# Performance work log

Measured on AMD Instinct MI355X. Metric: run time of the kernel, lower is better.

The kernel has to match this reference:

```python
import jax, jax.numpy as jnp
import numpy as np

N_NODES = 524288
N_EDGES = 786432
NUM_GRAPHS = 8192
NUM_NODE_TYPES = 16
NODE_DIM = 256
EDGE_DIM = 128
OUT_DIM = 1


def setup_inputs() -> dict:
    key = jax.random.key(0)
    ks = jax.random.split(key, 12)
    h_node = jax.random.uniform(ks[0], (N_NODES, NUM_NODE_TYPES), dtype=jnp.float32)
    pos_node = jax.random.normal(ks[1], (N_NODES, 3), dtype=jnp.float32)
    batch_node = jnp.sort(jax.random.randint(ks[2], (N_NODES,), 0, NUM_GRAPHS)).astype(jnp.int64)
    edge_index = jax.random.randint(ks[3], (2, N_EDGES), 0, N_NODES).astype(jnp.int64)
    batch_edge = jnp.sort(jax.random.randint(ks[4], (N_EDGES,), 0, NUM_GRAPHS)).astype(jnp.int64)
    s = 0.05
    W_node = jax.random.normal(ks[5], (NUM_NODE_TYPES, NODE_DIM), dtype=jnp.float32) * s
    W_edge = jax.random.normal(ks[6], (2 * NUM_NODE_TYPES, EDGE_DIM), dtype=jnp.float32) * s
    H = NODE_DIM + EDGE_DIM
    W1 = jax.random.normal(ks[7], (H, H), dtype=jnp.float32) * s
    b1 = jnp.zeros((H,), dtype=jnp.float32)
    W2 = jax.random.normal(ks[8], (H, OUT_DIM), dtype=jnp.float32) * s
    b2 = jnp.zeros((OUT_DIM,), dtype=jnp.float32)
    return {"h_node": h_node, "pos_node": pos_node, "batch_node": batch_node,
            "edge_index": edge_index, "batch_edge": batch_edge,
            "W_node": W_node, "W_edge": W_edge, "W1": W1, "b1": b1, "W2": W2, "b2": b2}


def _segment_mean(x, seg_ids, num_segments):
    # fused replacement for the original per-graph boolean-mask loop:
    # h[seg==k].mean(0) for all k, via one scatter-add + count normalize
    sums = jax.ops.segment_sum(x, seg_ids, num_segments=num_segments)
    cnts = jax.ops.segment_sum(jnp.ones((x.shape[0],), x.dtype), seg_ids, num_segments=num_segments)
    return sums / jnp.maximum(cnts, 1.0)[:, None]


def reference(h_node, pos_node, batch_node, edge_index, batch_edge,
              W_node, W_edge, W1, b1, W2, b2):
    # h_edge = cat(h_node[src], h_node[dst])  -> [E, 2*num_node_types]
    h_edge_raw = jnp.concatenate([h_node[edge_index[0]], h_node[edge_index[1]]], axis=-1)
    # num_timesteps == 0 path: plain embedders, no time embedding
    hn = h_node @ W_node          # [N, node_dim]
    he = h_edge_raw @ W_edge      # [E, edge_dim]
    # encoder treated as identity (NodeEdgeNet not in scope); pooling is the target op
    node_mean = _segment_mean(hn, batch_node, NUM_GRAPHS)  # [G, node_dim]
    edge_mean = _segment_mean(he, batch_edge, NUM_GRAPHS)  # [G, edge_dim]
    h_sub = jnp.concatenate([node_mean, edge_mean], axis=-1)  # [G, node_dim+edge_dim]
    # final MLP (num_layer=2): Linear -> ReLU -> Linear
    pred = jax.nn.relu(h_sub @ W1 + b1) @ W2 + b2  # [G, 1]
    return pred
```

## Files before the change

### kernel.cpp

```cpp
#include <hip/hip_runtime.h>

#define N_NODES_C   524288
#define N_EDGES_C   786432
#define NUM_GRAPHS_C 8192
#define NT 16
#define NODE_DIM_C 256
#define EDGE_DIM_C 128
#define HDIM 384
#define KC 48

#define FOLD_BLOCKS 72
#define NODE_BLOCKS 2048
#define EDGE_BLOCKS 16384
#define NODE_BASE   FOLD_BLOCKS
#define EDGE_BASE   (FOLD_BLOCKS + NODE_BLOCKS)
#define TOTAL_BLOCKS (FOLD_BLOCKS + NODE_BLOCKS + EDGE_BLOCKS)

#define WS_NM    0
#define WS_EM    524288
#define WS_WC    1572864
#define WS_NS    1646592
#define WS_BOFF  1679424
#define WS_ECNT  2203712
#define WS_REC   2236480

__device__ __forceinline__ void f4_add(float4& a, const float4 v) {
    a.x += v.x; a.y += v.y; a.z += v.z; a.w += v.w;
}

__device__ __forceinline__ void f4_shfl_xor_add(float4& a, int mask) {
    a.x += __shfl_xor(a.x, mask, 64);
    a.y += __shfl_xor(a.y, mask, 64);
    a.z += __shfl_xor(a.z, mask, 64);
    a.w += __shfl_xor(a.w, mask, 64);
}

__device__ __forceinline__ int lower_bound_i32(const int* __restrict__ a, int n, int key) {
    int lo = 0, hi = n;
    while (lo < hi) {
        int mid = (lo + hi) >> 1;
        if (a[mid] < key) lo = mid + 1; else hi = mid;
    }
    return lo;
}

__device__ __forceinline__ void wave_seg_bounds(const int* __restrict__ b, int n,
                                                int g, int lane, int& s, int& e) {
    int key = g + ((lane >= 32) ? 1 : 0);
    int lo = lower_bound_i32(b, n, key);
    s = __shfl(lo, 0, 64);
    e = __shfl(lo, 32, 64);
}

__global__ __launch_bounds__(256) void kr_build(
    const int* __restrict__ bnode, const int* __restrict__ bedge,
    const int* __restrict__ esrc, const int* __restrict__ edst,
    int* __restrict__ rec, int* __restrict__ binoff,
    int* __restrict__ ecnt, int* __restrict__ nstart, float* __restrict__ em) {
    int tid = threadIdx.x, blk = blockIdx.x;
    int i = blk * 256 + tid;
    {
        int g0 = bnode[i];
        int hi = (i + 1 < N_NODES_C) ? bnode[i + 1] : NUM_GRAPHS_C;
        if (i == 0) for (int g = 0; g <= g0; ++g) nstart[g] = 0;
        for (int g = g0 + 1; g <= hi; ++g) nstart[g] = i + 1;
    }
    if (tid < 128) em[blk * 128 + tid] = 0.f;

    int wave = tid >> 6, lane = tid & 63;
    int g = blk * 4 + wave;
    int s, e;
    wave_seg_bounds(bedge, N_EDGES_C, g, lane, s, e);
    if (lane == 0) ecnt[g] = e - s;

    __shared__ int lcnt[4][16];
    __shared__ int lcur[4][16];
    if (lane < 16) lcnt[wave][lane] = 0;
    for (int q = s + lane; q < e; q += 64) {
        int a = esrc[q];
        atomicAdd(&lcnt[wave][((a >> 16) << 1) + 0], 1);
        int b = edst[q];
        atomicAdd(&lcnt[wave][((b >> 16) << 1) + 1], 1);
    }
    int c = (lane < 16) ? lcnt[wave][lane] : 0;
    int incl = c;
    #pragma unroll
    for (int d = 1; d < 16; d <<= 1) {
        int v = __shfl_up(incl, d, 64);
        if (lane >= d) incl += v;
    }
    int excl = incl - c;
    if (lane < 16) {
        lcur[wave][lane] = excl;
        binoff[g * 16 + lane] = 2 * s + excl;
    }
    for (int q = s + lane; q < e; q += 64) {
        int a = esrc[q];
        int pa = atomicAdd(&lcur[wave][((a >> 16) << 1) + 0], 1);
        rec[2 * s + pa] = a;
        int b = edst[q];
        int pb = atomicAdd(&lcur[wave][((b >> 16) << 1) + 1], 1);
        rec[2 * s + pb] = b;
    }
}

__global__ __launch_bounds__(256) void km_mega(
    const float* __restrict__ h_node,
    const int* __restrict__ nstart, const int* __restrict__ binoff,
    const int* __restrict__ ecnt, const int* __restrict__ rec,
    const float* __restrict__ Wn, const float* __restrict__ We,
    const float* __restrict__ W1,
    float* __restrict__ nm, float* __restrict__ em, float* __restrict__ Wc) {
    int blk  = blockIdx.x;
    int wave = threadIdx.x >> 6;
    int lane = threadIdx.x & 63;
    const float4* h4 = (const float4*)h_node;
    const float4 z4 = make_float4(0.f, 0.f, 0.f, 0.f);

    if (blk < FOLD_BLOCKS) {
        int o = blk * 256 + threadIdx.x;
        if (o >= KC * HDIM) return;
        int k = o / HDIM, j = o % HDIM;
        float acc = 0.f;
        if (k < NT) {
            const float* wr = &Wn[k * NODE_DIM_C];
            #pragma unroll 16
            for (int kk = 0; kk < NODE_DIM_C; ++kk)
                acc = fmaf(wr[kk], W1[(size_t)kk * HDIM + j], acc);
        } else {
            const float* wr = &We[(k - NT) * EDGE_DIM_C];
            #pragma unroll 16
            for (int kk = 0; kk < EDGE_DIM_C; ++kk)
                acc = fmaf(wr[kk], W1[(size_t)(NODE_DIM_C + kk) * HDIM + j], acc);
        }
        Wc[o] = acc;
    } else if (blk < EDGE_BASE) {
        int r = blk - NODE_BASE;
        int s8 = r & 7;
        int g  = s8 * 1024 + (r >> 3) * 4 + wave;
        int s = nstart[g], e = nstart[g + 1];
        int row_off = lane >> 2;
        int quad    = lane & 3;
        float4 a0 = z4, a1 = z4;
        int i = s + row_off;
        for (; i + 16 < e; i += 32) {
            float4 v0 = h4[(size_t)i * 4 + quad];
            float4 v1 = h4[(size_t)(i + 16) * 4 + quad];
            f4_add(a0, v0);
            f4_add(a1, v1);
        }
        if (i < e) f4_add(a0, h4[(size_t)i * 4 + quad]);
        f4_add(a0, a1);
        f4_shfl_xor_add(a0, 4);
        f4_shfl_xor_add(a0, 8);
        f4_shfl_xor_add(a0, 16);
        f4_shfl_xor_add(a0, 32);
        if (row_off == 0) {
            float inv = 1.f / fmaxf((float)(e - s), 1.f);
            ((float4*)nm)[(size_t)g * 4 + quad] =
                make_float4(a0.x * inv, a0.y * inv, a0.z * inv, a0.w * inv);
        }
    } else {
        int r     = blk - EDGE_BASE;
        int slice = r & 7;
        int g     = (r >> 3) * 4 + wave;
        int b16   = g * 16 + slice * 2;
        int base0 = binoff[b16];
        int base1 = binoff[b16 + 1];
        int cnt   = ecnt[g];
        int end1  = (slice == 7) ? binoff[g * 16] + 2 * cnt : binoff[b16 + 2];
        int slot = lane >> 3;
        int p    = (lane >> 2) & 1;
        int quad = lane & 3;
        int st = p ? base1 : base0;
        int en = p ? end1  : base1;
        int cmax = max(base1 - base0, end1 - base1);
        int T = (cmax + 7) >> 3;
        float4 acc = z4;
        int i = st + slot;
        int idx = (i < en) ? rec[i] : -1;
        for (int t = 1; t < T; ++t) {
            int i2 = i + 8;
            int nx = (i2 < en) ? rec[i2] : -1;
            if (idx >= 0) f4_add(acc, h4[(size_t)idx * 4 + quad]);
            idx = nx; i = i2;
        }
        if (idx >= 0) f4_add(acc, h4[(size_t)idx * 4 + quad]);
        f4_shfl_xor_add(acc, 8);
        f4_shfl_xor_add(acc, 16);
        f4_shfl_xor_add(acc, 32);
        if (slot == 0) {
            float inv = 1.f / fmaxf((float)cnt, 1.f);
            float* dst = &em[(size_t)g * 32 + p * 16 + quad * 4];
            atomicAdd(dst + 0, acc.x * inv);
            atomicAdd(dst + 1, acc.y * inv);
            atomicAdd(dst + 2, acc.z * inv);
            atomicAdd(dst + 3, acc.w * inv);
        }
    }
}

#define GPB 16
__global__ __launch_bounds__(HDIM) void k3_mlp(
    const float* __restrict__ nm, const float* __restrict__ em,
    const float* __restrict__ Wc, const float* __restrict__ b1,
    const float* __restrict__ W2, const float* __restrict__ b2,
    float* __restrict__ pred) {
    int j = threadIdx.x;
    float wc[KC];
    #pragma unroll
    for (int k = 0; k < KC; ++k) wc[k] = Wc[k * HDIM + j];
    float b1j = b1[j], w2j = W2[j], b20 = b2[0];

    __shared__ float fs[GPB][KC];
    __shared__ float part[GPB][6];
    int g0 = blockIdx.x * GPB;
    #pragma unroll
    for (int t = j; t < GPB * KC; t += HDIM) {
        int g = t / KC, k = t % KC;
        fs[g][k] = (k < NT) ? nm[(size_t)(g0 + g) * NT + k]
                            : em[(size_t)(g0 + g) * 32 + (k - NT)];
    }
    __syncthreads();

    int wave = j >> 6, lane = j & 63;
    for (int g = 0; g < GPB; ++g) {
        float z = b1j;
        #pragma unroll
        for (int k = 0; k < KC; ++k) z = fmaf(fs[g][k], wc[k], z);
        z = fmaxf(z, 0.f);
        float p = z * w2j;
        #pragma unroll
        for (int off = 32; off > 0; off >>= 1) p += __shfl_down(p, off, 64);
        if (lane == 0) part[g][wave] = p;
    }
    __syncthreads();
    if (j < GPB) {
        float sacc = b20;
        #pragma unroll
        for (int w = 0; w < 6; ++w) sacc += part[j][w];
        pred[g0 + j] = sacc;
    }
}

extern "C" void kernel_launch(void* const* d_in, const int* in_sizes, int n_in,
                              void* d_out, int out_size, void* d_ws, size_t ws_size,
                              hipStream_t stream) {
    const float* h_node     = (const float*)d_in[0];
    const int*   batch_node = (const int*)d_in[2];
    const int*   edge_index = (const int*)d_in[3];
    const int*   batch_edge = (const int*)d_in[4];
    const float* W_node     = (const float*)d_in[5];
    const float* W_edge     = (const float*)d_in[6];
    const float* W1         = (const float*)d_in[7];
    const float* b1         = (const float*)d_in[8];
    const float* W2         = (const float*)d_in[9];
    const float* b2         = (const float*)d_in[10];
    float* pred = (float*)d_out;

    char* ws = (char*)d_ws;
    float* nm     = (float*)(ws + WS_NM);
    float* em     = (float*)(ws + WS_EM);
    float* Wc     = (float*)(ws + WS_WC);
    int*   nstart = (int*)(ws + WS_NS);
    int*   binoff = (int*)(ws + WS_BOFF);
    int*   ecnt   = (int*)(ws + WS_ECNT);
    int*   rec    = (int*)(ws + WS_REC);

    const int* esrc = edge_index;
    const int* edst = edge_index + N_EDGES_C;

    kr_build<<<NUM_GRAPHS_C / 4, 256, 0, stream>>>(
        batch_node, batch_edge, esrc, edst, rec, binoff, ecnt, nstart, em);
    km_mega <<<TOTAL_BLOCKS, 256, 0, stream>>>(
        h_node, nstart, binoff, ecnt, rec, W_node, W_edge, W1, nm, em, Wc);
    k3_mlp  <<<NUM_GRAPHS_C / GPB, HDIM, 0, stream>>>(
        nm, em, Wc, b1, W2, b2, pred);
}
```

Measured before the change: 154.5 us.

## Replace edge-mean atomics with per-slice partials reduced in MLP kernel

Each edge block now writes its per-slice partial sum with a plain float4 store into an 8-way partial buffer, so the float atomicAdds and the em zeroing are gone. The MLP kernel adds the eight partials and divides by the edge count. Per-slice bin bounds are packed into one int4 descriptor, so the edge path does a single load instead of several binoff and ecnt reads. The weight-fold work moves from the mega kernel into the build kernel. The cost is a larger workspace and extra reads in the MLP staging loop.

Result: faster. 150.0 us (-2.9%).

```diff
diff --git a/kernel.cpp b/kernel.cpp
--- a/kernel.cpp
+++ b/kernel.cpp
@@ -9,20 +9,21 @@
 #define HDIM 384
 #define KC 48
 
-#define FOLD_BLOCKS 72
+#define KR_GRAPH_BLOCKS 2048
+#define KR_FOLD_BLOCKS  72
+#define KR_BLOCKS (KR_GRAPH_BLOCKS + KR_FOLD_BLOCKS)
 #define NODE_BLOCKS 2048
 #define EDGE_BLOCKS 16384
-#define NODE_BASE   FOLD_BLOCKS
-#define EDGE_BASE   (FOLD_BLOCKS + NODE_BLOCKS)
-#define TOTAL_BLOCKS (FOLD_BLOCKS + NODE_BLOCKS + EDGE_BLOCKS)
+#define EDGE_BASE   NODE_BLOCKS
+#define KM_BLOCKS   (NODE_BLOCKS + EDGE_BLOCKS)
 
 #define WS_NM    0
-#define WS_EM    524288
-#define WS_WC    1572864
-#define WS_NS    1646592
-#define WS_BOFF  1679424
-#define WS_ECNT  2203712
-#define WS_REC   2236480
+#define WS_EM8   524288
+#define WS_WC    8912896
+#define WS_NS    8986624
+#define WS_DESC  9019456
+#define WS_ECNT  10068032
+#define WS_REC   10100800
 
 __device__ __forceinline__ void f4_add(float4& a, const float4 v) {
     a.x += v.x; a.y += v.y; a.z += v.z; a.w += v.w;
@@ -55,70 +56,14 @@
 __global__ __launch_bounds__(256) void kr_build(
     const int* __restrict__ bnode, const int* __restrict__ bedge,
     const int* __restrict__ esrc, const int* __restrict__ edst,
-    int* __restrict__ rec, int* __restrict__ binoff,
-    int* __restrict__ ecnt, int* __restrict__ nstart, float* __restrict__ em) {
-    int tid = threadIdx.x, blk = blockIdx.x;
-    int i = blk * 256 + tid;
-    {
-        int g0 = bnode[i];
-        int hi = (i + 1 < N_NODES_C) ? bnode[i + 1] : NUM_GRAPHS_C;
-        if (i == 0) for (int g = 0; g <= g0; ++g) nstart[g] = 0;
-        for (int g = g0 + 1; g <= hi; ++g) nstart[g] = i + 1;
-    }
-    if (tid < 128) em[blk * 128 + tid] = 0.f;
-
-    int wave = tid >> 6, lane = tid & 63;
-    int g = blk * 4 + wave;
-    int s, e;
-    wave_seg_bounds(bedge, N_EDGES_C, g, lane, s, e);
-    if (lane == 0) ecnt[g] = e - s;
-
-    __shared__ int lcnt[4][16];
-    __shared__ int lcur[4][16];
-    if (lane < 16) lcnt[wave][lane] = 0;
-    for (int q = s + lane; q < e; q += 64) {
-        int a = esrc[q];
-        atomicAdd(&lcnt[wave][((a >> 16) << 1) + 0], 1);
-        int b = edst[q];
-        atomicAdd(&lcnt[wave][((b >> 16) << 1) + 1], 1);
-    }
-    int c = (lane < 16) ? lcnt[wave][lane] : 0;
-    int incl = c;
-    #pragma unroll
-    for (int d = 1; d < 16; d <<= 1) {
-        int v = __shfl_up(incl, d, 64);
-        if (lane >= d) incl += v;
-    }
-    int excl = incl - c;
-    if (lane < 16) {
-        lcur[wave][lane] = excl;
-        binoff[g * 16 + lane] = 2 * s + excl;
-    }
-    for (int q = s + lane; q < e; q += 64) {
-        int a = esrc[q];
-        int pa = atomicAdd(&lcur[wave][((a >> 16) << 1) + 0], 1);
-        rec[2 * s + pa] = a;
-        int b = edst[q];
-        int pb = atomicAdd(&lcur[wave][((b >> 16) << 1) + 1], 1);
-        rec[2 * s + pb] = b;
-    }
-}
-
-__global__ __launch_bounds__(256) void km_mega(
-    const float* __restrict__ h_node,
-    const int* __restrict__ nstart, const int* __restrict__ binoff,
-    const int* __restrict__ ecnt, const int* __restrict__ rec,
     const float* __restrict__ Wn, const float* __restrict__ We,
     const float* __restrict__ W1,
-    float* __restrict__ nm, float* __restrict__ em, float* __restrict__ Wc) {
-    int blk  = blockIdx.x;
-    int wave = threadIdx.x >> 6;
-    int lane = threadIdx.x & 63;
-    const float4* h4 = (const float4*)h_node;
-    const float4 z4 = make_float4(0.f, 0.f, 0.f, 0.f);
-
-    if (blk < FOLD_BLOCKS) {
-        int o = blk * 256 + threadIdx.x;
+    int* __restrict__ rec, int4* __restrict__ desc,
+    int* __restrict__ ecnt, int* __restrict__ nstart, float* __restrict__ Wc) {
+    int tid = threadIdx.x, blk = blockIdx.x;
+
+    if (blk >= KR_GRAPH_BLOCKS) {
+        int o = (blk - KR_GRAPH_BLOCKS) * 256 + tid;
         if (o >= KC * HDIM) return;
         int k = o / HDIM, j = o % HDIM;
         float acc = 0.f;
@@ -134,10 +79,76 @@
                 acc = fmaf(wr[kk], W1[(size_t)(NODE_DIM_C + kk) * HDIM + j], acc);
         }
         Wc[o] = acc;
-    } else if (blk < EDGE_BASE) {
-        int r = blk - NODE_BASE;
-        int s8 = r & 7;
-        int g  = s8 * 1024 + (r >> 3) * 4 + wave;
+        return;
+    }
+
+    int i = blk * 256 + tid;
+    {
+        int g0 = bnode[i];
+        int hi = (i + 1 < N_NODES_C) ? bnode[i + 1] : NUM_GRAPHS_C;
+        if (i == 0) for (int g = 0; g <= g0; ++g) nstart[g] = 0;
+        for (int g = g0 + 1; g <= hi; ++g) nstart[g] = i + 1;
+    }
+
+    int wave = tid >> 6, lane = tid & 63;
+    int g = blk * 4 + wave;
+    int s, e;
+    wave_seg_bounds(bedge, N_EDGES_C, g, lane, s, e);
+    int cnt = e - s;
+    if (lane == 0) ecnt[g] = cnt;
+
+    __shared__ int lcnt[4][16];
+    __shared__ int lcur[4][16];
+    if (lane < 16) lcnt[wave][lane] = 0;
+    for (int q = s + lane; q < e; q += 64) {
+        int a = esrc[q];
+        atomicAdd(&lcnt[wave][((a >> 16) << 1) + 0], 1);
+        int b = edst[q];
+        atomicAdd(&lcnt[wave][((b >> 16) << 1) + 1], 1);
+    }
+    int c = (lane < 16) ? lcnt[wave][lane] : 0;
+    int incl = c;
+    #pragma unroll
+    for (int d = 1; d < 16; d <<= 1) {
+        int v = __shfl_up(incl, d, 64);
+        if (lane >= d) incl += v;
+    }
+    int excl = incl - c;
+    if (lane < 16) lcur[wave][lane] = excl;
+    int i0 = (lane < 8) ? 2 * lane : 0;
+    int i1 = (lane < 8) ? 2 * lane + 1 : 0;
+    int i2 = (lane < 7) ? 2 * lane + 2 : 0;
+    int b0 = __shfl(excl, i0, 64);
+    int b1 = __shfl(excl, i1, 64);
+    int e1 = __shfl(excl, i2, 64);
+    if (lane < 8) {
+        int e1a = (lane == 7) ? 2 * s + 2 * cnt : 2 * s + e1;
+        desc[(g << 3) + lane] = make_int4(2 * s + b0, 2 * s + b1, e1a, cnt);
+    }
+    for (int q = s + lane; q < e; q += 64) {
+        int a = esrc[q];
+        int pa = atomicAdd(&lcur[wave][((a >> 16) << 1) + 0], 1);
+        rec[2 * s + pa] = a;
+        int b = edst[q];
+        int pb = atomicAdd(&lcur[wave][((b >> 16) << 1) + 1], 1);
+        rec[2 * s + pb] = b;
+    }
+}
+
+__global__ __launch_bounds__(256) void km_mega(
+    const float* __restrict__ h_node,
+    const int* __restrict__ nstart, const int4* __restrict__ desc,
+    const int* __restrict__ rec,
+    float* __restrict__ nm, float* __restrict__ em8) {
+    int blk  = blockIdx.x;
+    int wave = threadIdx.x >> 6;
+    int lane = threadIdx.x & 63;
+    const float4* h4 = (const float4*)h_node;
+    const float4 z4 = make_float4(0.f, 0.f, 0.f, 0.f);
+
+    if (blk < EDGE_BASE) {
+        int s8 = blk & 7;
+        int g  = s8 * 1024 + (blk >> 3) * 4 + wave;
         int s = nstart[g], e = nstart[g + 1];
         int row_off = lane >> 2;
         int quad    = lane & 3;
@@ -164,17 +175,13 @@
         int r     = blk - EDGE_BASE;
         int slice = r & 7;
         int g     = (r >> 3) * 4 + wave;
-        int b16   = g * 16 + slice * 2;
-        int base0 = binoff[b16];
-        int base1 = binoff[b16 + 1];
-        int cnt   = ecnt[g];
-        int end1  = (slice == 7) ? binoff[g * 16] + 2 * cnt : binoff[b16 + 2];
+        int4 d    = desc[(g << 3) + slice];
         int slot = lane >> 3;
         int p    = (lane >> 2) & 1;
         int quad = lane & 3;
-        int st = p ? base1 : base0;
-        int en = p ? end1  : base1;
-        int cmax = max(base1 - base0, end1 - base1);
+        int st = p ? d.y : d.x;
+        int en = p ? d.z : d.y;
+        int cmax = max(d.y - d.x, d.z - d.y);
         int T = (cmax + 7) >> 3;
         float4 acc = z4;
         int i = st + slot;
@@ -190,19 +197,15 @@
         f4_shfl_xor_add(acc, 16);
         f4_shfl_xor_add(acc, 32);
         if (slot == 0) {
-            float inv = 1.f / fmaxf((float)cnt, 1.f);
-            float* dst = &em[(size_t)g * 32 + p * 16 + quad * 4];
-            atomicAdd(dst + 0, acc.x * inv);
-            atomicAdd(dst + 1, acc.y * inv);
-            atomicAdd(dst + 2, acc.z * inv);
-            atomicAdd(dst + 3, acc.w * inv);
+            ((float4*)em8)[((size_t)(g * 8 + slice)) * 8 + p * 4 + quad] = acc;
         }
     }
 }
 
 #define GPB 16
 __global__ __launch_bounds__(HDIM) void k3_mlp(
-    const float* __restrict__ nm, const float* __restrict__ em,
+    const float* __restrict__ nm, const float* __restrict__ em8,
+    const int* __restrict__ ecnt,
     const float* __restrict__ Wc, const float* __restrict__ b1,
     const float* __restrict__ W2, const float* __restrict__ b2,
     float* __restrict__ pred) {
@@ -215,11 +218,20 @@
     __shared__ float fs[GPB][KC];
     __shared__ float part[GPB][6];
     int g0 = blockIdx.x * GPB;
-    #pragma unroll
     for (int t = j; t < GPB * KC; t += HDIM) {
         int g = t / KC, k = t % KC;
-        fs[g][k] = (k < NT) ? nm[(size_t)(g0 + g) * NT + k]
-                            : em[(size_t)(g0 + g) * 32 + (k - NT)];
+        int G = g0 + g;
+        float val;
+        if (k < NT) {
+            val = nm[(size_t)G * NT + k];
+        } else {
+            float ssum = 0.f;
+            #pragma unroll
+            for (int s = 0; s < 8; ++s)
+                ssum += em8[((size_t)(G * 8 + s)) * 32 + (k - NT)];
+            val = ssum / fmaxf((float)ecnt[G], 1.f);
+        }
+        fs[g][k] = val;
     }
     __syncthreads();
 
@@ -260,20 +272,21 @@
 
     char* ws = (char*)d_ws;
     float* nm     = (float*)(ws + WS_NM);
-    float* em     = (float*)(ws + WS_EM);
+    float* em8    = (float*)(ws + WS_EM8);
     float* Wc     = (float*)(ws + WS_WC);
     int*   nstart = (int*)(ws + WS_NS);
-    int*   binoff = (int*)(ws + WS_BOFF);
+    int4*  desc   = (int4*)(ws + WS_DESC);
     int*   ecnt   = (int*)(ws + WS_ECNT);
     int*   rec    = (int*)(ws + WS_REC);
 
     const int* esrc = edge_index;
     const int* edst = edge_index + N_EDGES_C;
 
-    kr_build<<<NUM_GRAPHS_C / 4, 256, 0, stream>>>(
-        batch_node, batch_edge, esrc, edst, rec, binoff, ecnt, nstart, em);
-    km_mega <<<TOTAL_BLOCKS, 256, 0, stream>>>(
-        h_node, nstart, binoff, ecnt, rec, W_node, W_edge, W1, nm, em, Wc);
+    kr_build<<<KR_BLOCKS, 256, 0, stream>>>(
+        batch_node, batch_edge, esrc, edst, W_node, W_edge, W1,
+        rec, desc, ecnt, nstart, Wc);
+    km_mega <<<KM_BLOCKS, 256, 0, stream>>>(
+        h_node, nstart, desc, rec, nm, em8);
     k3_mlp  <<<NUM_GRAPHS_C / GPB, HDIM, 0, stream>>>(
-        nm, em, Wc, b1, W2, b2, pred);
-}
+        nm, em8, ecnt, Wc, b1, W2, b2, pred);
+}
```
